# Performance work log

Hardware: AMD Instinct MI355X
Metric: run time of the kernel (lower is better)

## Reference

```python
import jax, jax.numpy as jnp
import numpy as np

B, N, F, S, OUT = 8, 12000, 128, 16, 128

def setup_inputs() -> dict:
    key = jax.random.key(0)
    k1, k2, k3, k4 = jax.random.split(key, 4)
    x = jax.random.normal(k1, (B, N, F), dtype=jnp.float32)
    # Linear(in_c*spiral_size, out_c): weight [out, in], bias [out]
    bound = 1.0 / np.sqrt(F * S)
    W = jax.random.uniform(k2, (OUT, F * S), dtype=jnp.float32, minval=-bound, maxval=bound)
    b = jax.random.uniform(k3, (OUT,), dtype=jnp.float32, minval=-bound, maxval=bound)
    spiral_adj = jax.random.randint(k4, (1, N, S), 0, N, dtype=jnp.int32)
    zero_padding = jnp.ones((1, N, 1), dtype=jnp.float32)
    return {"x": x, "W": W, "b": b, "spiral_adj": spiral_adj, "zero_padding": zero_padding}

def reference(x, W, b, spiral_adj, zero_padding):
    # x: [B, N, F]; spiral_adj: [1, N, S] vertex indices shared across batch
    idx = spiral_adj[0]                         # [N, S]
    spirals = x[:, idx, :]                      # [B, N, S, F] gather along vertex dim
    bsz, npts, s, f = spirals.shape
    spirals = spirals.reshape(bsz, npts, s * f)  # [B, N, S*F]
    out = jnp.einsum('bnk,ok->bno', spirals, W) + b  # [B, N, OUT]
    out = jax.nn.relu(out)
    return out * zero_padding
```

## Files before the change

kernel.cpp:

```cpp
#include <hip/hip_runtime.h>

#define BATCH 8
#define NPTS  12000
#define FDIM  128
#define SDIM  16
#define ODIM  128
#define KDIM  (SDIM * FDIM)
#define MTOT  (BATCH * NPTS)

#define BM 128
#define BK 64

#define NTILES 94
#define XELEMS (BATCH * NPTS * FDIM)
#define WELEMS (ODIM * KDIM)
#define XBYTES ((size_t)XELEMS * 2)
#define WBYTES ((size_t)WELEMS * 2)
#define XN4    (XELEMS / 4)
#define WN4    (WELEMS / 4)

typedef __bf16 bf16x4 __attribute__((ext_vector_type(4)));
typedef __bf16 bf16x8 __attribute__((ext_vector_type(8)));
typedef float  f32x4  __attribute__((ext_vector_type(4)));
typedef float  f32x8  __attribute__((ext_vector_type(8)));

#define AS1(p) ((const __attribute__((address_space(1))) void*)(p))
#define AS3(p) ((__attribute__((address_space(3))) void*)(p))

__global__ __launch_bounds__(256)
void cvt_f32_bf16(const float* __restrict__ x, const float* __restrict__ W,
                  __bf16* __restrict__ xb, __bf16* __restrict__ Wb) {
    int i = blockIdx.x * blockDim.x + threadIdx.x;
    const int stride = gridDim.x * blockDim.x;
    for (; i < XN4 + WN4; i += stride) {
        const float* src; __bf16* dst; int j;
        if (i < XN4) { src = x; dst = xb; j = i; }
        else         { src = W; dst = Wb; j = i - XN4; }
        const float4 v = reinterpret_cast<const float4*>(src)[j];
        bf16x4 h;
        h[0] = (__bf16)v.x; h[1] = (__bf16)v.y;
        h[2] = (__bf16)v.z; h[3] = (__bf16)v.w;
        reinterpret_cast<bf16x4*>(dst)[j] = h;
    }
}

__global__ __launch_bounds__(256, 2)
void spiral_gemm_bf16(const __bf16* __restrict__ xb,
                      const __bf16* __restrict__ Wb,
                      const float*  __restrict__ bias,
                      const int*    __restrict__ idx,
                      const float*  __restrict__ zp,
                      float*        __restrict__ out)
{
    __shared__ __bf16 As[2][BM * BK];
    __shared__ __bf16 Ws[2][ODIM * BK];
    __shared__ int    idxS[BM * SDIM];

    const int tid   = threadIdx.x;
    const int wave  = tid >> 6;
    const int lane  = tid & 63;
    const int batch = blockIdx.x & 7;
    const int n0    = (blockIdx.x >> 3) * BM;

    const int lrow8 = lane >> 3;
    const int clog  = (lane & 7) ^ lrow8;

    const __bf16* xbase = xb + (size_t)batch * (NPTS * FDIM);

    {
        const int row  = tid >> 1, half = tid & 1;
        const int n    = n0 + row;
        const int nrow = n < NPTS ? n : NPTS - 1;
        const int4* s4 = reinterpret_cast<const int4*>(idx + nrow * SDIM + half * 8);
        int4* d4       = reinterpret_cast<int4*>(&idxS[row * SDIM + half * 8]);
        d4[0] = s4[0];
        d4[1] = s4[1];
    }
    __syncthreads();

    int rrow[4];
#pragma unroll
    for (int p = 0; p < 4; ++p) rrow[p] = (p * 4 + wave) * 8 + lrow8;

    int gCur[4], gNext[4];
#pragma unroll
    for (int p = 0; p < 4; ++p) gCur[p] = idxS[rrow[p] * SDIM + 0];

    const int wm   = (wave >> 1) * 64;
    const int wn   = (wave & 1) * 64;
    const int lrow = lane & 15;
    const int quad = lane >> 4;

    f32x4 acc[4][4];
#pragma unroll
    for (int i = 0; i < 4; ++i)
#pragma unroll
        for (int j = 0; j < 4; ++j)
            acc[i][j] = f32x4{0.f, 0.f, 0.f, 0.f};

    auto dmaA4 = [&](int buf, int f0, const int* g) {
#pragma unroll
        for (int p = 0; p < 4; ++p) {
            const int r0 = (p * 4 + wave) * 8;
            const __bf16* ga = xbase + (size_t)g[p] * FDIM + f0 + clog * 8;
            __builtin_amdgcn_global_load_lds(AS1(ga), AS3(&As[buf][r0 * BK]), 16, 0, 0);
        }
    };
    auto dmaW4 = [&](int buf, int ktn) {
#pragma unroll
        for (int p = 0; p < 4; ++p) {
            const int r0 = (p * 4 + wave) * 8;
            const __bf16* gw = Wb + (size_t)(r0 + lrow8) * KDIM + ktn * BK + clog * 8;
            __builtin_amdgcn_global_load_lds(AS1(gw), AS3(&Ws[buf][r0 * BK]), 16, 0, 0);
        }
    };

    auto compute_kk = [&](int buf, int kk) {
        const int ph = (kk * 4 + quad) ^ (lrow & 7);
        bf16x8 a[4], b[4];
#pragma unroll
        for (int i = 0; i < 4; ++i)
            a[i] = *reinterpret_cast<const bf16x8*>(
                &As[buf][(wm + i * 16 + lrow) * BK + ph * 8]);
#pragma unroll
        for (int j = 0; j < 4; ++j)
            b[j] = *reinterpret_cast<const bf16x8*>(
                &Ws[buf][(wn + j * 16 + lrow) * BK + ph * 8]);
        __builtin_amdgcn_s_setprio(1);
#pragma unroll
        for (int i = 0; i < 4; ++i)
#pragma unroll
            for (int j = 0; j < 4; ++j)
                acc[i][j] = __builtin_amdgcn_mfma_f32_16x16x32_bf16(
                    a[i], b[j], acc[i][j], 0, 0, 0);
        __builtin_amdgcn_s_setprio(0);
    };

    dmaA4(0, 0, gCur);
    dmaW4(0, 0);

    for (int u = 0; u < 16; ++u) {
        dmaA4(1, BK, gCur);
        asm volatile("s_waitcnt vmcnt(4)" ::: "memory");
        asm volatile("s_barrier" ::: "memory");
        compute_kk(0, 0);
        asm volatile("s_barrier" ::: "memory");
        dmaW4(1, 2 * u + 1);
        if (u < 15) {
#pragma unroll
            for (int p = 0; p < 4; ++p)
                gNext[p] = idxS[rrow[p] * SDIM + u + 1];
        }
        compute_kk(0, 1);
        asm volatile("s_barrier" ::: "memory");

        if (u < 15) {
            dmaA4(0, 0, gNext);
            asm volatile("s_waitcnt vmcnt(4)" ::: "memory");
            asm volatile("s_barrier" ::: "memory");
            compute_kk(1, 0);
            asm volatile("s_barrier" ::: "memory");
            dmaW4(0, 2 * u + 2);
            compute_kk(1, 1);
            asm volatile("s_barrier" ::: "memory");
#pragma unroll
            for (int p = 0; p < 4; ++p) gCur[p] = gNext[p];
        } else {
            asm volatile("s_waitcnt vmcnt(0)" ::: "memory");
            asm volatile("s_barrier" ::: "memory");
            compute_kk(1, 0);
            asm volatile("s_barrier" ::: "memory");
            compute_kk(1, 1);
            asm volatile("s_barrier" ::: "memory");
        }
    }

#pragma unroll
    for (int i = 0; i < 4; ++i) {
#pragma unroll
        for (int r = 0; r < 4; ++r) {
            const int row = wm + i * 16 + quad * 4 + r;
            const int n   = n0 + row;
            if (n < NPTS) {
                const float z = zp[n];
                float* orow   = out + ((size_t)batch * NPTS + n) * ODIM;
#pragma unroll
                for (int j = 0; j < 4; ++j) {
                    const int col = wn + j * 16 + lrow;
                    float v = acc[i][j][r] + bias[col];
                    v = fmaxf(v, 0.f);
                    orow[col] = v * z;
                }
            }
        }
    }
}

#define LDA 72
__global__ __launch_bounds__(256, 2)
void spiral_gemm_fp32(const float* __restrict__ x, const float* __restrict__ W,
                      const float* __restrict__ bias, const int* __restrict__ idx,
                      const float* __restrict__ zp, float* __restrict__ out)
{
    __shared__ __bf16 Asf[BM * LDA];
    __shared__ __bf16 Wsf[ODIM * LDA];
    const int tid = threadIdx.x, wave = tid >> 6, lane = tid & 63;
    const int m0 = blockIdx.x * BM;
    const int srow = tid >> 3, schunk = tid & 7;
    int a_n[4]; const float* a_xb[4];
#pragma unroll
    for (int p = 0; p < 4; ++p) {
        int m = m0 + srow + p * 32, bb = m / NPTS;
        a_n[p] = m - bb * NPTS; a_xb[p] = x + (size_t)bb * (NPTS * FDIM);
    }
    f32x4 acc[4][4];
#pragma unroll
    for (int i = 0; i < 4; ++i)
#pragma unroll
        for (int j = 0; j < 4; ++j) acc[i][j] = f32x4{0.f,0.f,0.f,0.f};
    const int wm = (wave >> 1) * 64, wn = (wave & 1) * 64;
    const int lrow = lane & 15, quad = lane >> 4;
    for (int kt = 0; kt < KDIM / BK; ++kt) {
        const int s = kt >> 1, f0 = (kt & 1) * BK;
        __syncthreads();
#pragma unroll
        for (int p = 0; p < 4; ++p) {
            const int r = srow + p * 32;
            const int g = idx[a_n[p] * SDIM + s];
            const f32x8 v = *reinterpret_cast<const f32x8*>(
                a_xb[p] + (size_t)g * FDIM + f0 + schunk * 8);
            bf16x8 h;
#pragma unroll
            for (int e = 0; e < 8; ++e) h[e] = (__bf16)v[e];
            *reinterpret_cast<bf16x8*>(&Asf[r * LDA + schunk * 8]) = h;
            const f32x8 w = *reinterpret_cast<const f32x8*>(
                W + (size_t)r * KDIM + kt * BK + schunk * 8);
            bf16x8 hw;
#pragma unroll
            for (int e = 0; e < 8; ++e) hw[e] = (__bf16)w[e];
            *reinterpret_cast<bf16x8*>(&Wsf[r * LDA + schunk * 8]) = hw;
        }
        __syncthreads();
#pragma unroll
        for (int kk = 0; kk < 2; ++kk) {
            const int koff = kk * 32 + quad * 8;
            bf16x8 a[4], b[4];
#pragma unroll
            for (int i = 0; i < 4; ++i)
                a[i] = *reinterpret_cast<const bf16x8*>(&Asf[(wm + i*16 + lrow)*LDA + koff]);
#pragma unroll
            for (int j = 0; j < 4; ++j)
                b[j] = *reinterpret_cast<const bf16x8*>(&Wsf[(wn + j*16 + lrow)*LDA + koff]);
#pragma unroll
            for (int i = 0; i < 4; ++i)
#pragma unroll
                for (int j = 0; j < 4; ++j)
                    acc[i][j] = __builtin_amdgcn_mfma_f32_16x16x32_bf16(a[i], b[j], acc[i][j], 0,0,0);
        }
    }
#pragma unroll
    for (int i = 0; i < 4; ++i)
#pragma unroll
        for (int r = 0; r < 4; ++r) {
            const int row = wm + i * 16 + quad * 4 + r;
            const int m = m0 + row, bb = m / NPTS, nnn = m - bb * NPTS;
            const float z = zp[nnn];
            float* orow = out + (size_t)m * ODIM;
#pragma unroll
            for (int j = 0; j < 4; ++j) {
                const int col = wn + j * 16 + lrow;
                float v = acc[i][j][r] + bias[col];
                orow[col] = fmaxf(v, 0.f) * z;
            }
        }
}

extern "C" void kernel_launch(void* const* d_in, const int* in_sizes, int n_in,
                              void* d_out, int out_size, void* d_ws, size_t ws_size,
                              hipStream_t stream) {
    const float* x    = (const float*)d_in[0];
    const float* W    = (const float*)d_in[1];
    const float* bias = (const float*)d_in[2];
    const int*   idx  = (const int*)d_in[3];
    const float* zp   = (const float*)d_in[4];
    float*       out  = (float*)d_out;

    if (ws_size >= XBYTES + WBYTES) {
        __bf16* xb = (__bf16*)d_ws;
        __bf16* Wb = (__bf16*)((char*)d_ws + XBYTES);
        cvt_f32_bf16<<<dim3(1024), dim3(256), 0, stream>>>(x, W, xb, Wb);
        spiral_gemm_bf16<<<dim3(BATCH * NTILES), dim3(256), 0, stream>>>(
            xb, Wb, bias, idx, zp, out);
    } else {
        spiral_gemm_fp32<<<dim3(MTOT / BM), dim3(256), 0, stream>>>(
            x, W, bias, idx, zp, out);
    }
}
```

Baseline: 169.2 us.

## Load W fragments directly into registers instead of staging through LDS

```diff
diff --git a/kernel.cpp b/kernel.cpp
--- a/kernel.cpp
+++ b/kernel.cpp
@@ -44,7 +44,7 @@
     }
 }
 
-__global__ __launch_bounds__(256, 2)
+__global__ __launch_bounds__(256, 3)
 void spiral_gemm_bf16(const __bf16* __restrict__ xb,
                       const __bf16* __restrict__ Wb,
                       const float*  __restrict__ bias,
@@ -53,7 +53,6 @@
                       float*        __restrict__ out)
 {
     __shared__ __bf16 As[2][BM * BK];
-    __shared__ __bf16 Ws[2][ODIM * BK];
     __shared__ int    idxS[BM * SDIM];
 
     const int tid   = threadIdx.x;
@@ -106,72 +105,69 @@
             __builtin_amdgcn_global_load_lds(AS1(ga), AS3(&As[buf][r0 * BK]), 16, 0, 0);
         }
     };
-    auto dmaW4 = [&](int buf, int ktn) {
-#pragma unroll
-        for (int p = 0; p < 4; ++p) {
-            const int r0 = (p * 4 + wave) * 8;
-            const __bf16* gw = Wb + (size_t)(r0 + lrow8) * KDIM + ktn * BK + clog * 8;
-            __builtin_amdgcn_global_load_lds(AS1(gw), AS3(&Ws[buf][r0 * BK]), 16, 0, 0);
-        }
+
+    const __bf16* wlane = Wb + (size_t)(wn + lrow) * KDIM + quad * 8;
+    auto bload = [&](bf16x8 (&bb)[2][4], int kt) {
+#pragma unroll
+        for (int kk = 0; kk < 2; ++kk)
+#pragma unroll
+            for (int j = 0; j < 4; ++j)
+                bb[kk][j] = *reinterpret_cast<const bf16x8*>(
+                    wlane + (size_t)j * 16 * KDIM + kt * BK + kk * 32);
     };
 
-    auto compute_kk = [&](int buf, int kk) {
-        const int ph = (kk * 4 + quad) ^ (lrow & 7);
-        bf16x8 a[4], b[4];
-#pragma unroll
-        for (int i = 0; i < 4; ++i)
-            a[i] = *reinterpret_cast<const bf16x8*>(
-                &As[buf][(wm + i * 16 + lrow) * BK + ph * 8]);
-#pragma unroll
-        for (int j = 0; j < 4; ++j)
-            b[j] = *reinterpret_cast<const bf16x8*>(
-                &Ws[buf][(wn + j * 16 + lrow) * BK + ph * 8]);
-        __builtin_amdgcn_s_setprio(1);
-#pragma unroll
-        for (int i = 0; i < 4; ++i)
-#pragma unroll
-            for (int j = 0; j < 4; ++j)
-                acc[i][j] = __builtin_amdgcn_mfma_f32_16x16x32_bf16(
-                    a[i], b[j], acc[i][j], 0, 0, 0);
-        __builtin_amdgcn_s_setprio(0);
+    auto compute = [&](int buf, const bf16x8 (&bb)[2][4]) {
+#pragma unroll
+        for (int kk = 0; kk < 2; ++kk) {
+            const int ph = (kk * 4 + quad) ^ (lrow & 7);
+            bf16x8 a[4];
+#pragma unroll
+            for (int i = 0; i < 4; ++i)
+                a[i] = *reinterpret_cast<const bf16x8*>(
+                    &As[buf][(wm + i * 16 + lrow) * BK + ph * 8]);
+#pragma unroll
+            for (int i = 0; i < 4; ++i)
+#pragma unroll
+                for (int j = 0; j < 4; ++j)
+                    acc[i][j] = __builtin_amdgcn_mfma_f32_16x16x32_bf16(
+                        a[i], bb[kk][j], acc[i][j], 0, 0, 0);
+        }
     };
 
+    bf16x8 bA[2][4], bB[2][4];
+
+    bload(bA, 0);
+    __builtin_amdgcn_sched_barrier(0);
     dmaA4(0, 0, gCur);
-    dmaW4(0, 0);
 
     for (int u = 0; u < 16; ++u) {
+        bload(bB, 2 * u + 1);
+        __builtin_amdgcn_sched_barrier(0);
         dmaA4(1, BK, gCur);
-        asm volatile("s_waitcnt vmcnt(4)" ::: "memory");
+        asm volatile("s_waitcnt vmcnt(12)" ::: "memory");
         asm volatile("s_barrier" ::: "memory");
-        compute_kk(0, 0);
-        asm volatile("s_barrier" ::: "memory");
-        dmaW4(1, 2 * u + 1);
         if (u < 15) {
 #pragma unroll
             for (int p = 0; p < 4; ++p)
                 gNext[p] = idxS[rrow[p] * SDIM + u + 1];
         }
-        compute_kk(0, 1);
+        compute(0, bA);
         asm volatile("s_barrier" ::: "memory");
 
         if (u < 15) {
+            bload(bA, 2 * u + 2);
+            __builtin_amdgcn_sched_barrier(0);
             dmaA4(0, 0, gNext);
-            asm volatile("s_waitcnt vmcnt(4)" ::: "memory");
+            asm volatile("s_waitcnt vmcnt(12)" ::: "memory");
             asm volatile("s_barrier" ::: "memory");
-            compute_kk(1, 0);
-            asm volatile("s_barrier" ::: "memory");
-            dmaW4(0, 2 * u + 2);
-            compute_kk(1, 1);
+            compute(1, bB);
             asm volatile("s_barrier" ::: "memory");
 #pragma unroll
             for (int p = 0; p < 4; ++p) gCur[p] = gNext[p];
         } else {
             asm volatile("s_waitcnt vmcnt(0)" ::: "memory");
             asm volatile("s_barrier" ::: "memory");
-            compute_kk(1, 0);
-            asm volatile("s_barrier" ::: "memory");
-            compute_kk(1, 1);
-            asm volatile("s_barrier" ::: "memory");
+            compute(1, bB);
         }
     }
 
```

Measured after the change: 208.8 us. 23.4% more time.
